# Kernel tuning notes

Hardware: AMD Instinct MI355X
Metric: run time of the kernel (lower is better)

The kernel has to match this reference:

```python
import jax, jax.numpy as jnp
import numpy as np

D_MODEL = 1024
N_HEADS = 16
D_K = D_MODEL // N_HEADS
LOCAL_WINDOW = 128
GLOBAL_TOKENS = 16


def sparse_mask(seq_len):
    i = jnp.arange(seq_len)[:, None]
    j = jnp.arange(seq_len)[None, :]
    local = jnp.abs(i - j) <= LOCAL_WINDOW
    glob = (i < GLOBAL_TOKENS) | (j < GLOBAL_TOKENS)
    causal = j <= i
    return ((local | glob) & causal)[None, None]  # [1,1,S,S]


def setup_inputs() -> dict:
    key = jax.random.key(0)
    ks = jax.random.split(key, 11)
    B, S = 2, 2048
    std = 1.0 / np.sqrt(D_MODEL)
    inp = {
        'query': jax.random.normal(ks[0], (B, S, D_MODEL), jnp.float32),
        'key': jax.random.normal(ks[1], (B, S, D_MODEL), jnp.float32),
        'value': jax.random.normal(ks[2], (B, S, D_MODEL), jnp.float32),
        'w_q': jax.random.normal(ks[3], (D_MODEL, D_MODEL), jnp.float32) * std,
        'b_q': jnp.zeros((D_MODEL,), jnp.float32),
        'w_k': jax.random.normal(ks[4], (D_MODEL, D_MODEL), jnp.float32) * std,
        'b_k': jnp.zeros((D_MODEL,), jnp.float32),
        'w_v': jax.random.normal(ks[5], (D_MODEL, D_MODEL), jnp.float32) * std,
        'b_v': jnp.zeros((D_MODEL,), jnp.float32),
        'w_o': jax.random.normal(ks[6], (D_MODEL, D_MODEL), jnp.float32) * std,
        'b_o': jnp.zeros((D_MODEL,), jnp.float32),
    }
    return inp


def reference(query, key, value, w_q, b_q, w_k, b_k, w_v, b_v, w_o, b_o):
    B, S, _ = query.shape
    # project and split heads -> [B,H,S,d_k]
    def proj(x, w, b):
        y = x @ w.T + b
        return y.reshape(B, S, N_HEADS, D_K).transpose(0, 2, 1, 3)
    q = proj(query, w_q, b_q)
    k = proj(key, w_k, b_k)
    v = proj(value, w_v, b_v)
    scores = jnp.einsum('bhqd,bhkd->bhqk', q, k) / np.sqrt(D_K).astype(np.float32)
    mask = sparse_mask(S)
    scores = jnp.where(mask, scores, -jnp.inf)
    attn = jax.nn.softmax(scores, axis=-1)
    out = jnp.einsum('bhqk,bhkd->bhqd', attn, v)
    out = out.transpose(0, 2, 1, 3).reshape(B, S, D_MODEL)
    return out @ w_o.T + b_o
```

## Files before the change

### kernel.cpp

```cpp
#include <hip/hip_runtime.h>

typedef unsigned short u16;
typedef u16 u16x8 __attribute__((ext_vector_type(8)));
typedef __bf16 bf16x8 __attribute__((ext_vector_type(8)));
typedef float f32x4 __attribute__((ext_vector_type(4)));

#define MFMA16 __builtin_amdgcn_mfma_f32_16x16x32_bf16

__device__ __forceinline__ u16 f2bf(float f) {
  unsigned u = __builtin_bit_cast(unsigned, f);
  u += 0x7FFFu + ((u >> 16) & 1u);
  return (u16)(u >> 16);
}

__device__ __forceinline__ int swz(int row, int bcol) {
  return row * 128 + (bcol ^ ((row & 7) << 4));
}

__device__ __forceinline__ void gl16(const u16* g, u16* l) {
  __builtin_amdgcn_global_load_lds(
      (const __attribute__((address_space(1))) unsigned int*)g,
      (__attribute__((address_space(3))) unsigned int*)l, 16, 0, 0);
}

__device__ __forceinline__ void BARR() {
  asm volatile("" ::: "memory");
  __builtin_amdgcn_s_barrier();
  asm volatile("" ::: "memory");
}
#define VMCNT(n) asm volatile("s_waitcnt vmcnt(" #n ")" ::: "memory")

__global__ __launch_bounds__(256)
void cast7(const float* __restrict__ a0, const float* __restrict__ a1,
           const float* __restrict__ a2, const float* __restrict__ a3,
           const float* __restrict__ a4, const float* __restrict__ a5,
           const float* __restrict__ a6, u16* __restrict__ ws) {
  const int y = blockIdx.y;
  const float* s;
  u16* d;
  int n;
  switch (y) {
    case 0: s = a0; d = ws + 4194304; n = 4194304; break;
    case 1: s = a1; d = ws + 8388608; n = 4194304; break;
    case 2: s = a2; d = ws + 12582912; n = 4194304; break;
    case 3: s = a3; d = ws + 0; n = 1048576; break;
    case 4: s = a4; d = ws + 1048576; n = 1048576; break;
    case 5: s = a5; d = ws + 2097152; n = 1048576; break;
    default: s = a6; d = ws + 3145728; n = 1048576; break;
  }
  const int i = (blockIdx.x * 256 + threadIdx.x) * 8;
  if (i >= n) return;
  float4 v0 = *(const float4*)(s + i);
  float4 v1 = *(const float4*)(s + i + 4);
  u16x8 p = {f2bf(v0.x), f2bf(v0.y), f2bf(v0.z), f2bf(v0.w),
             f2bf(v1.x), f2bf(v1.y), f2bf(v1.z), f2bf(v1.w)};
  *(u16x8*)(d + i) = p;
}

#define STGA(tt, c)                                                         \
  gl16(A + (m0 + (c)*64 + (w << 3) + (lane >> 3)) * 1024 + (tt)*64 +        \
           (((lane & 7) ^ (lane >> 3)) << 3),                               \
       (u16*)(sb + (((tt)&1) << 16) + (c)*8192 + (w << 10)))
#define STGB(tt, c)                                                         \
  gl16(B + (n0 + (c)*64 + (w << 3) + (lane >> 3)) * 1024 + (tt)*64 +        \
           (((lane & 7) ^ (lane >> 3)) << 3),                               \
       (u16*)(sb + (((tt)&1) << 16) + 32768 + (c)*8192 + (w << 10)))

__global__ __launch_bounds__(512)
void qkv_gemm256(const u16* __restrict__ ws_in, const float* __restrict__ c0,
                 const float* __restrict__ c1, const float* __restrict__ c2,
                 u16* __restrict__ o0, u16* __restrict__ o1,
                 u16* __restrict__ o2) {
  const int bid = blockIdx.x;
  const int s = (bid & 7) * 24 + (bid >> 3);
  const int z = s >> 6;
  const int rem = s & 63;
  const int m0 = (rem >> 2) << 8;
  const int n0 = (rem & 3) << 8;

  const u16* __restrict__ A = ws_in + 4194304 + z * 4194304;
  const u16* __restrict__ B = ws_in + z * 1048576;
  const float* Bi = (z == 0) ? c0 : (z == 1) ? c1 : c2;
  u16* O = (z == 0) ? o0 : (z == 1) ? o1 : o2;

  const int tid = threadIdx.x, lane = tid & 63, w = tid >> 6;
  const int wm = w >> 2, wn = w & 3;
  const int r = lane & 15, g = lane >> 4;

  __shared__ u16 SH[65536];
  char* sb = (char*)SH;

  f32x4 acc[8][4] = {};
  bf16x8 af[2][4], bf[2][4];

  const int colr0 = (g * 16) ^ ((r & 7) << 4);
  const int colr1 = (64 + g * 16) ^ ((r & 7) << 4);
  const int rowAb = (wm * 128 + r) * 128;
  const int rowBb = 32768 + (wn * 64 + r) * 128;

#define LDA(half)                                                           \
  _Pragma("unroll") for (int m = 0; m < 4; ++m) {                           \
    char* p = sb + bo + rowAb + ((half)*64 + m * 16) * 128;                 \
    af[0][m] = __builtin_bit_cast(bf16x8, *(const u16x8*)(p + colr0));      \
    af[1][m] = __builtin_bit_cast(bf16x8, *(const u16x8*)(p + colr1));      \
  }
#define LDB(n)                                                              \
  {                                                                         \
    char* p = sb + bo + rowBb + (n)*16 * 128;                               \
    bf[0][n] = __builtin_bit_cast(bf16x8, *(const u16x8*)(p + colr0));      \
    bf[1][n] = __builtin_bit_cast(bf16x8, *(const u16x8*)(p + colr1));      \
  }
#define FMAH(h)                                                             \
  __builtin_amdgcn_s_setprio(1);                                            \
  _Pragma("unroll") for (int m = 0; m < 4; ++m)                             \
  _Pragma("unroll") for (int n = 0; n < 4; ++n) {                           \
    acc[(h)*4 + m][n] = MFMA16(af[0][m], bf[0][n], acc[(h)*4 + m][n], 0, 0, \
                               0);                                          \
    acc[(h)*4 + m][n] = MFMA16(af[1][m], bf[1][n], acc[(h)*4 + m][n], 0, 0, \
                               0);                                          \
  }                                                                         \
  __builtin_amdgcn_s_setprio(0);

#pragma unroll
  for (int c = 0; c < 4; ++c) STGB(0, c);
#pragma unroll
  for (int c = 0; c < 4; ++c) STGA(0, c);
  VMCNT(0);
  __builtin_amdgcn_s_barrier();
  asm volatile("" ::: "memory");

  for (int t = 0; t < 16; ++t) {
    const int bo = (t & 1) << 16;
    if (t < 15) { STGB(t + 1, 0); STGB(t + 1, 1); STGB(t + 1, 2); STGB(t + 1, 3); }
    LDA(0);
    LDB(0); LDB(1); LDB(2); LDB(3);
    FMAH(0);
    if (t < 15) { VMCNT(4); } else { VMCNT(0); }
    BARR();
    if (t < 15) { STGA(t + 1, 0); STGA(t + 1, 2); STGA(t + 1, 1); STGA(t + 1, 3); }
    LDA(1);
    FMAH(1);
    if (t < 15) { VMCNT(2); }
    BARR();
  }

#pragma unroll
  for (int n = 0; n < 4; ++n) {
    const int gn = n0 + wn * 64 + n * 16 + r;
    const int hh = gn >> 6, d = gn & 63;
    const float bv = Bi[gn];
#pragma unroll
    for (int m = 0; m < 8; ++m) {
#pragma unroll
      for (int q = 0; q < 4; ++q) {
        int gm = m0 + wm * 128 + m * 16 + g * 4 + q;
        int bb = gm >> 11, sIdx = gm & 2047;
        O[((bb * 16 + hh) * 2048 + sIdx) * 64 + d] = f2bf(acc[m][n][q] + bv);
      }
    }
  }
#undef LDA
#undef LDB
#undef FMAH
}

#define OSTGA(tt, c, j)                                                     \
  gl16(Ain + (m0 + (c)*64 + (w << 4) + (j)*8 + (lane >> 3)) * 1024 +        \
           (tt)*64 + (((lane & 7) ^ (lane >> 3)) << 3),                     \
       (u16*)(sb + (((tt)&1) << 15) + (c)*8192 + (w << 11) + ((j) << 10)))
#define OSTGB(tt, c, j)                                                     \
  gl16(W + (n0 + (c)*64 + (w << 4) + (j)*8 + (lane >> 3)) * 1024 +          \
           (tt)*64 + (((lane & 7) ^ (lane >> 3)) << 3),                     \
       (u16*)(sb + (((tt)&1) << 15) + 16384 + (c)*8192 + (w << 11) +        \
              ((j) << 10)))

__global__ __launch_bounds__(256)
void out_gemm_p(const u16* __restrict__ Ain, const u16* __restrict__ W,
                const float* __restrict__ Bi, float* __restrict__ C) {
  const int bid = blockIdx.x;
  const int s = (bid & 7) * 32 + (bid >> 3);
  const int m0 = (s >> 3) << 7, n0 = (s & 7) << 7;

  const int tid = threadIdx.x, lane = tid & 63, w = tid >> 6;
  const int wm = w >> 1, wn = w & 1;
  const int r = lane & 15, g = lane >> 4;

  __shared__ u16 SH[32768];
  char* sb = (char*)SH;

  f32x4 acc[4][4] = {};
  bf16x8 af[2][4], bf[2][4];

  const int colr0 = (g * 16) ^ ((r & 7) << 4);
  const int colr1 = (64 + g * 16) ^ ((r & 7) << 4);
  const int rowAb = (wm * 64 + r) * 128;
  const int rowBb = 16384 + (wn * 64 + r) * 128;

#define OLDA()                                                              \
  _Pragma("unroll") for (int m = 0; m < 4; ++m) {                           \
    char* p = sb + bo + rowAb + m * 16 * 128;                               \
    af[0][m] = __builtin_bit_cast(bf16x8, *(const u16x8*)(p + colr0));      \
    af[1][m] = __builtin_bit_cast(bf16x8, *(const u16x8*)(p + colr1));      \
  }
#define OLDB(n)                                                             \
  {                                                                         \
    char* p = sb + bo + rowBb + (n)*16 * 128;                               \
    bf[0][n] = __builtin_bit_cast(bf16x8, *(const u16x8*)(p + colr0));      \
    bf[1][n] = __builtin_bit_cast(bf16x8, *(const u16x8*)(p + colr1));      \
  }
#define OFMA(nh)                                                            \
  __builtin_amdgcn_s_setprio(1);                                            \
  _Pragma("unroll") for (int m = 0; m < 4; ++m)                             \
  _Pragma("unroll") for (int n = 0; n < 2; ++n) {                           \
    acc[m][(nh)*2 + n] =                                                    \
        MFMA16(af[0][m], bf[0][(nh)*2 + n], acc[m][(nh)*2 + n], 0, 0, 0);   \
    acc[m][(nh)*2 + n] =                                                    \
        MFMA16(af[1][m], bf[1][(nh)*2 + n], acc[m][(nh)*2 + n], 0, 0, 0);   \
  }                                                                         \
  __builtin_amdgcn_s_setprio(0);

#pragma unroll
  for (int c = 0; c < 2; ++c) { OSTGA(0, c, 0); OSTGA(0, c, 1); }
#pragma unroll
  for (int c = 0; c < 2; ++c) { OSTGB(0, c, 0); OSTGB(0, c, 1); }
#pragma unroll
  for (int c = 0; c < 2; ++c) { OSTGA(1, c, 0); OSTGA(1, c, 1); }
  VMCNT(4);
  __builtin_amdgcn_s_barrier();
  asm volatile("" ::: "memory");

  for (int t = 0; t < 16; ++t) {
    const int bo = (t & 1) << 15;
    if (t < 15) { OSTGB(t + 1, 0, 0); OSTGB(t + 1, 0, 1); OSTGB(t + 1, 1, 0); OSTGB(t + 1, 1, 1); }
    OLDA();
    OLDB(0); OLDB(1);
    OFMA(0);
    BARR();
    if (t < 14) { OSTGA(t + 2, 0, 0); OSTGA(t + 2, 0, 1); OSTGA(t + 2, 1, 0); OSTGA(t + 2, 1, 1); }
    OLDB(2); OLDB(3);
    OFMA(1);
    if (t < 14) { VMCNT(4); } else if (t == 14) { VMCNT(0); }
    BARR();
  }

#pragma unroll
  for (int m = 0; m < 4; ++m) {
#pragma unroll
    for (int n = 0; n < 4; ++n) {
      int gn = n0 + wn * 64 + n * 16 + r;
      float bv = Bi[gn];
#pragma unroll
      for (int q = 0; q < 4; ++q) {
        int gm = m0 + wm * 64 + m * 16 + g * 4 + q;
        C[gm * 1024 + gn] = acc[m][n][q] + bv;
      }
    }
  }
#undef OLDA
#undef OLDB
#undef OFMA
}

__global__ __launch_bounds__(256)
void attn_kernel(const u16* __restrict__ Q, const u16* __restrict__ K,
                 const u16* __restrict__ V, u16* __restrict__ O) {
  const int qt = blockIdx.x, h = blockIdx.y, b = blockIdx.z;
  const int tid = threadIdx.x, lane = tid & 63, w = tid >> 6;
  const int r = lane & 15, g = lane >> 4;
  const int q0 = qt * 64;
  const int base = (b * 16 + h) * 131072;
  const u16* Qb = Q + base;
  const u16* Kb = K + base;
  const u16* Vb = V + base;

  __shared__ u16 Ks[64 * 64];
  __shared__ u16 Vt[64 * 64];
  __shared__ u16 Pl[4608];

  bf16x8 qf[2];
  {
    const u16* qp = Qb + (q0 + w * 16 + r) * 64 + g * 8;
    qf[0] = __builtin_bit_cast(bf16x8, *(const u16x8*)qp);
    qf[1] = __builtin_bit_cast(bf16x8, *(const u16x8*)(qp + 32));
  }

  f32x4 acc[4] = {};
  float m_run[4] = {-1e30f, -1e30f, -1e30f, -1e30f};
  float l_run[4] = {};

  const int nt = (qt <= 3) ? (qt + 1) : 4;
  const int srow = tid >> 3, sc = (tid & 7) * 8;

  for (int tix = 0; tix < nt; ++tix) {
    const int t = (tix == 0) ? 0 : ((qt <= 3) ? tix : (qt - 3 + tix));
    const int j0 = t * 64;
    __syncthreads();
#pragma unroll
    for (int i = 0; i < 2; ++i) {
      int row = i * 32 + srow;
      u16x8 kv = *(const u16x8*)(Kb + (j0 + row) * 64 + sc);
      *(u16x8*)((char*)Ks + swz(row, sc * 2)) = kv;
      u16x8 vv = *(const u16x8*)(Vb + (j0 + row) * 64 + sc);
#pragma unroll
      for (int qq = 0; qq < 8; ++qq) {
        int d = sc + qq;
        *(u16*)((char*)Vt + d * 128 + ((2 * row) ^ ((d & 7) << 4))) = vv[qq];
      }
    }
    __syncthreads();

    f32x4 S[4] = {};
#pragma unroll
    for (int kk = 0; kk < 2; ++kk)
#pragma unroll
      for (int n = 0; n < 4; ++n) {
        bf16x8 kf = __builtin_bit_cast(
            bf16x8,
            *(const u16x8*)((char*)Ks + swz(n * 16 + r, kk * 64 + g * 16)));
        S[n] = MFMA16(qf[kk], kf, S[n], 0, 0, 0);
      }

    float mloc[4] = {-1e30f, -1e30f, -1e30f, -1e30f};
#pragma unroll
    for (int n = 0; n < 4; ++n) {
      int j = j0 + n * 16 + r;
#pragma unroll
      for (int q = 0; q < 4; ++q) {
        int i = q0 + w * 16 + g * 4 + q;
        bool ok = (j <= i) && (((i - j) <= 128) || (j < 16));
        float s = ok ? S[n][q] * 0.125f : -1e30f;
        S[n][q] = s;
        mloc[q] = fmaxf(mloc[q], s);
      }
    }
#pragma unroll
    for (int q = 0; q < 4; ++q)
#pragma unroll
      for (int off = 1; off < 16; off <<= 1)
        mloc[q] = fmaxf(mloc[q], __shfl_xor(mloc[q], off));

    float alpha[4], rsum[4] = {};
#pragma unroll
    for (int q = 0; q < 4; ++q) {
      float mn = fmaxf(m_run[q], mloc[q]);
      alpha[q] = __expf(m_run[q] - mn);
      m_run[q] = mn;
    }
#pragma unroll
    for (int n = 0; n < 4; ++n)
#pragma unroll
      for (int q = 0; q < 4; ++q) {
        float p = __expf(S[n][q] - m_run[q]);
        S[n][q] = p;
        rsum[q] += p;
      }
#pragma unroll
    for (int q = 0; q < 4; ++q) {
#pragma unroll
      for (int off = 1; off < 16; off <<= 1)
        rsum[q] += __shfl_xor(rsum[q], off);
      l_run[q] = l_run[q] * alpha[q] + rsum[q];
    }
#pragma unroll
    for (int n = 0; n < 4; ++n) {
      acc[n][0] *= alpha[0];
      acc[n][1] *= alpha[1];
      acc[n][2] *= alpha[2];
      acc[n][3] *= alpha[3];
    }

#pragma unroll
    for (int n = 0; n < 4; ++n)
#pragma unroll
      for (int q = 0; q < 4; ++q)
        *((u16*)((char*)Pl + w * 2304 + (g * 4 + q) * 144) + (n * 16 + r)) =
            f2bf(S[n][q]);

#pragma unroll
    for (int kk = 0; kk < 2; ++kk) {
      bf16x8 pf = __builtin_bit_cast(
          bf16x8,
          *(const u16x8*)((char*)Pl + w * 2304 + r * 144 + kk * 64 + g * 16));
#pragma unroll
      for (int n = 0; n < 4; ++n) {
        bf16x8 vf = __builtin_bit_cast(
            bf16x8,
            *(const u16x8*)((char*)Vt + swz(n * 16 + r, kk * 64 + g * 16)));
        acc[n] = MFMA16(pf, vf, acc[n], 0, 0, 0);
      }
    }
  }

#pragma unroll
  for (int n = 0; n < 4; ++n)
#pragma unroll
    for (int q = 0; q < 4; ++q) {
      int s = q0 + w * 16 + g * 4 + q;
      int d = n * 16 + r;
      O[(b * 2048 + s) * 1024 + h * 64 + d] = f2bf(acc[n][q] / l_run[q]);
    }
}

extern "C" void kernel_launch(void* const* d_in, const int* in_sizes, int n_in,
                              void* d_out, int out_size, void* d_ws,
                              size_t ws_size, hipStream_t stream) {
  const float* b_q = (const float*)d_in[4];
  const float* b_k = (const float*)d_in[6];
  const float* b_v = (const float*)d_in[8];
  const float* b_o = (const float*)d_in[10];

  u16* ws = (u16*)d_ws;
  u16* Qw = ws + 16777216;
  u16* Kw = ws + 20971520;
  u16* Vw = ws + 25165824;
  u16* Aw = ws + 4194304;

  cast7<<<dim3(2048, 7), dim3(256), 0, stream>>>(
      (const float*)d_in[0], (const float*)d_in[1], (const float*)d_in[2],
      (const float*)d_in[3], (const float*)d_in[5], (const float*)d_in[7],
      (const float*)d_in[9], ws);
  qkv_gemm256<<<dim3(192), dim3(512), 0, stream>>>(ws, b_q, b_k, b_v, Qw, Kw,
                                                   Vw);
  attn_kernel<<<dim3(32, 16, 2), dim3(256), 0, stream>>>(Qw, Kw, Vw, Aw);
  out_gemm_p<<<dim3(256), dim3(256), 0, stream>>>(Aw, ws + 3145728, b_o,
                                                  (float*)d_out);
}
```

Measured before the change: 96.04 us.

## Switch QKV GEMM to shared 128x128 tile core and flatten cast grid

Replaces the 256x256-tile, 512-thread QKV projection GEMM with a 128x128-tile, 256-thread kernel that reuses the output-projection GEMM's inner loop, now factored into a shared core128 function. The launch grows from 192 to 768 blocks, which should fill the MI355X's compute units better and allow more than one block per CU, since each block uses half the LDS. The trade-off is lower data reuse per tile, so global and L2 traffic go up. The cast kernel also moves to a flat 1D grid, which removes the idle threads the old version had in the weight-matrix rows.

```diff
diff --git a/kernel.cpp b/kernel.cpp
--- a/kernel.cpp
+++ b/kernel.cpp
@@ -31,137 +31,30 @@
 #define VMCNT(n) asm volatile("s_waitcnt vmcnt(" #n ")" ::: "memory")
 
 __global__ __launch_bounds__(256)
-void cast7(const float* __restrict__ a0, const float* __restrict__ a1,
-           const float* __restrict__ a2, const float* __restrict__ a3,
-           const float* __restrict__ a4, const float* __restrict__ a5,
-           const float* __restrict__ a6, u16* __restrict__ ws) {
-  const int y = blockIdx.y;
+void cast_all(const float* __restrict__ q, const float* __restrict__ k,
+              const float* __restrict__ v, const float* __restrict__ wq,
+              const float* __restrict__ wk, const float* __restrict__ wv,
+              const float* __restrict__ wo, u16* __restrict__ ws) {
+  const long i = ((long)blockIdx.x * 256 + threadIdx.x) * 8;
   const float* s;
   u16* d;
-  int n;
-  switch (y) {
-    case 0: s = a0; d = ws + 4194304; n = 4194304; break;
-    case 1: s = a1; d = ws + 8388608; n = 4194304; break;
-    case 2: s = a2; d = ws + 12582912; n = 4194304; break;
-    case 3: s = a3; d = ws + 0; n = 1048576; break;
-    case 4: s = a4; d = ws + 1048576; n = 1048576; break;
-    case 5: s = a5; d = ws + 2097152; n = 1048576; break;
-    default: s = a6; d = ws + 3145728; n = 1048576; break;
-  }
-  const int i = (blockIdx.x * 256 + threadIdx.x) * 8;
-  if (i >= n) return;
-  float4 v0 = *(const float4*)(s + i);
-  float4 v1 = *(const float4*)(s + i + 4);
+  if (i < 12582912) {
+    const int seg = (int)(i >> 22);
+    const float* xs = (seg == 0) ? q : (seg == 1) ? k : v;
+    s = xs + (i & 4194303);
+    d = ws + 4194304 + i;
+  } else {
+    const long j = i - 12582912;
+    const int seg = (int)(j >> 20);
+    const float* wsrc = (seg == 0) ? wq : (seg == 1) ? wk : (seg == 2) ? wv : wo;
+    s = wsrc + (j & 1048575);
+    d = ws + j;
+  }
+  float4 v0 = *(const float4*)s;
+  float4 v1 = *(const float4*)(s + 4);
   u16x8 p = {f2bf(v0.x), f2bf(v0.y), f2bf(v0.z), f2bf(v0.w),
              f2bf(v1.x), f2bf(v1.y), f2bf(v1.z), f2bf(v1.w)};
-  *(u16x8*)(d + i) = p;
-}
-
-#define STGA(tt, c)                                                         \
-  gl16(A + (m0 + (c)*64 + (w << 3) + (lane >> 3)) * 1024 + (tt)*64 +        \
-           (((lane & 7) ^ (lane >> 3)) << 3),                               \
-       (u16*)(sb + (((tt)&1) << 16) + (c)*8192 + (w << 10)))
-#define STGB(tt, c)                                                         \
-  gl16(B + (n0 + (c)*64 + (w << 3) + (lane >> 3)) * 1024 + (tt)*64 +        \
-           (((lane & 7) ^ (lane >> 3)) << 3),                               \
-       (u16*)(sb + (((tt)&1) << 16) + 32768 + (c)*8192 + (w << 10)))
-
-__global__ __launch_bounds__(512)
-void qkv_gemm256(const u16* __restrict__ ws_in, const float* __restrict__ c0,
-                 const float* __restrict__ c1, const float* __restrict__ c2,
-                 u16* __restrict__ o0, u16* __restrict__ o1,
-                 u16* __restrict__ o2) {
-  const int bid = blockIdx.x;
-  const int s = (bid & 7) * 24 + (bid >> 3);
-  const int z = s >> 6;
-  const int rem = s & 63;
-  const int m0 = (rem >> 2) << 8;
-  const int n0 = (rem & 3) << 8;
-
-  const u16* __restrict__ A = ws_in + 4194304 + z * 4194304;
-  const u16* __restrict__ B = ws_in + z * 1048576;
-  const float* Bi = (z == 0) ? c0 : (z == 1) ? c1 : c2;
-  u16* O = (z == 0) ? o0 : (z == 1) ? o1 : o2;
-
-  const int tid = threadIdx.x, lane = tid & 63, w = tid >> 6;
-  const int wm = w >> 2, wn = w & 3;
-  const int r = lane & 15, g = lane >> 4;
-
-  __shared__ u16 SH[65536];
-  char* sb = (char*)SH;
-
-  f32x4 acc[8][4] = {};
-  bf16x8 af[2][4], bf[2][4];
-
-  const int colr0 = (g * 16) ^ ((r & 7) << 4);
-  const int colr1 = (64 + g * 16) ^ ((r & 7) << 4);
-  const int rowAb = (wm * 128 + r) * 128;
-  const int rowBb = 32768 + (wn * 64 + r) * 128;
-
-#define LDA(half)                                                           \
-  _Pragma("unroll") for (int m = 0; m < 4; ++m) {                           \
-    char* p = sb + bo + rowAb + ((half)*64 + m * 16) * 128;                 \
-    af[0][m] = __builtin_bit_cast(bf16x8, *(const u16x8*)(p + colr0));      \
-    af[1][m] = __builtin_bit_cast(bf16x8, *(const u16x8*)(p + colr1));      \
-  }
-#define LDB(n)                                                              \
-  {                                                                         \
-    char* p = sb + bo + rowBb + (n)*16 * 128;                               \
-    bf[0][n] = __builtin_bit_cast(bf16x8, *(const u16x8*)(p + colr0));      \
-    bf[1][n] = __builtin_bit_cast(bf16x8, *(const u16x8*)(p + colr1));      \
-  }
-#define FMAH(h)                                                             \
-  __builtin_amdgcn_s_setprio(1);                                            \
-  _Pragma("unroll") for (int m = 0; m < 4; ++m)                             \
-  _Pragma("unroll") for (int n = 0; n < 4; ++n) {                           \
-    acc[(h)*4 + m][n] = MFMA16(af[0][m], bf[0][n], acc[(h)*4 + m][n], 0, 0, \
-                               0);                                          \
-    acc[(h)*4 + m][n] = MFMA16(af[1][m], bf[1][n], acc[(h)*4 + m][n], 0, 0, \
-                               0);                                          \
-  }                                                                         \
-  __builtin_amdgcn_s_setprio(0);
-
-#pragma unroll
-  for (int c = 0; c < 4; ++c) STGB(0, c);
-#pragma unroll
-  for (int c = 0; c < 4; ++c) STGA(0, c);
-  VMCNT(0);
-  __builtin_amdgcn_s_barrier();
-  asm volatile("" ::: "memory");
-
-  for (int t = 0; t < 16; ++t) {
-    const int bo = (t & 1) << 16;
-    if (t < 15) { STGB(t + 1, 0); STGB(t + 1, 1); STGB(t + 1, 2); STGB(t + 1, 3); }
-    LDA(0);
-    LDB(0); LDB(1); LDB(2); LDB(3);
-    FMAH(0);
-    if (t < 15) { VMCNT(4); } else { VMCNT(0); }
-    BARR();
-    if (t < 15) { STGA(t + 1, 0); STGA(t + 1, 2); STGA(t + 1, 1); STGA(t + 1, 3); }
-    LDA(1);
-    FMAH(1);
-    if (t < 15) { VMCNT(2); }
-    BARR();
-  }
-
-#pragma unroll
-  for (int n = 0; n < 4; ++n) {
-    const int gn = n0 + wn * 64 + n * 16 + r;
-    const int hh = gn >> 6, d = gn & 63;
-    const float bv = Bi[gn];
-#pragma unroll
-    for (int m = 0; m < 8; ++m) {
-#pragma unroll
-      for (int q = 0; q < 4; ++q) {
-        int gm = m0 + wm * 128 + m * 16 + g * 4 + q;
-        int bb = gm >> 11, sIdx = gm & 2047;
-        O[((bb * 16 + hh) * 2048 + sIdx) * 64 + d] = f2bf(acc[m][n][q] + bv);
-      }
-    }
-  }
-#undef LDA
-#undef LDB
-#undef FMAH
+  *(u16x8*)d = p;
 }
 
 #define OSTGA(tt, c, j)                                                     \
@@ -173,29 +66,6 @@
            (tt)*64 + (((lane & 7) ^ (lane >> 3)) << 3),                     \
        (u16*)(sb + (((tt)&1) << 15) + 16384 + (c)*8192 + (w << 11) +        \
               ((j) << 10)))
-
-__global__ __launch_bounds__(256)
-void out_gemm_p(const u16* __restrict__ Ain, const u16* __restrict__ W,
-                const float* __restrict__ Bi, float* __restrict__ C) {
-  const int bid = blockIdx.x;
-  const int s = (bid & 7) * 32 + (bid >> 3);
-  const int m0 = (s >> 3) << 7, n0 = (s & 7) << 7;
-
-  const int tid = threadIdx.x, lane = tid & 63, w = tid >> 6;
-  const int wm = w >> 1, wn = w & 1;
-  const int r = lane & 15, g = lane >> 4;
-
-  __shared__ u16 SH[32768];
-  char* sb = (char*)SH;
-
-  f32x4 acc[4][4] = {};
-  bf16x8 af[2][4], bf[2][4];
-
-  const int colr0 = (g * 16) ^ ((r & 7) << 4);
-  const int colr1 = (64 + g * 16) ^ ((r & 7) << 4);
-  const int rowAb = (wm * 64 + r) * 128;
-  const int rowBb = 16384 + (wn * 64 + r) * 128;
-
 #define OLDA()                                                              \
   _Pragma("unroll") for (int m = 0; m < 4; ++m) {                           \
     char* p = sb + bo + rowAb + m * 16 * 128;                               \
@@ -218,6 +88,20 @@
         MFMA16(af[1][m], bf[1][(nh)*2 + n], acc[m][(nh)*2 + n], 0, 0, 0);   \
   }                                                                         \
   __builtin_amdgcn_s_setprio(0);
+
+__device__ __forceinline__ void core128(const u16* __restrict__ Ain,
+                                        const u16* __restrict__ W, int m0,
+                                        int n0, char* sb,
+                                        f32x4 (&acc)[4][4]) {
+  const int tid = threadIdx.x, lane = tid & 63, w = tid >> 6;
+  const int wm = w >> 1, wn = w & 1;
+  const int r = lane & 15, g = lane >> 4;
+  bf16x8 af[2][4], bf[2][4];
+
+  const int colr0 = (g * 16) ^ ((r & 7) << 4);
+  const int colr1 = (64 + g * 16) ^ ((r & 7) << 4);
+  const int rowAb = (wm * 64 + r) * 128;
+  const int rowBb = 16384 + (wn * 64 + r) * 128;
 
 #pragma unroll
   for (int c = 0; c < 2; ++c) { OSTGA(0, c, 0); OSTGA(0, c, 1); }
@@ -242,6 +126,63 @@
     if (t < 14) { VMCNT(4); } else if (t == 14) { VMCNT(0); }
     BARR();
   }
+}
+
+__global__ __launch_bounds__(256)
+void qkv_gemm128(const u16* __restrict__ ws_in, const float* __restrict__ c0,
+                 const float* __restrict__ c1, const float* __restrict__ c2,
+                 u16* __restrict__ o0, u16* __restrict__ o1,
+                 u16* __restrict__ o2) {
+  const int bid = blockIdx.x;
+  const int s = (bid & 7) * 96 + (bid >> 3);
+  const int z = s >> 8;
+  const int rem = s & 255;
+  const int m0 = (rem >> 3) << 7, n0 = (rem & 7) << 7;
+
+  const u16* __restrict__ Ain = ws_in + 4194304 + z * 4194304;
+  const u16* __restrict__ W = ws_in + z * 1048576;
+  const float* Bi = (z == 0) ? c0 : (z == 1) ? c1 : c2;
+  u16* O = (z == 0) ? o0 : (z == 1) ? o1 : o2;
+
+  const int tid = threadIdx.x, lane = tid & 63, w = tid >> 6;
+  const int wm = w >> 1, wn = w & 1;
+  const int r = lane & 15, g = lane >> 4;
+
+  __shared__ u16 SH[32768];
+  f32x4 acc[4][4] = {};
+  core128(Ain, W, m0, n0, (char*)SH, acc);
+
+#pragma unroll
+  for (int n = 0; n < 4; ++n) {
+    const int gn = n0 + wn * 64 + n * 16 + r;
+    const int hh = gn >> 6, d = gn & 63;
+    const float bv = Bi[gn];
+#pragma unroll
+    for (int m = 0; m < 4; ++m) {
+#pragma unroll
+      for (int q = 0; q < 4; ++q) {
+        int gm = m0 + wm * 64 + m * 16 + g * 4 + q;
+        int bb = gm >> 11, sIdx = gm & 2047;
+        O[((bb * 16 + hh) * 2048 + sIdx) * 64 + d] = f2bf(acc[m][n][q] + bv);
+      }
+    }
+  }
+}
+
+__global__ __launch_bounds__(256)
+void out_gemm_p(const u16* __restrict__ Ain2, const u16* __restrict__ W2,
+                const float* __restrict__ Bi, float* __restrict__ C) {
+  const int bid = blockIdx.x;
+  const int s = (bid & 7) * 32 + (bid >> 3);
+  const int m0 = (s >> 3) << 7, n0 = (s & 7) << 7;
+
+  const int tid = threadIdx.x, lane = tid & 63, w = tid >> 6;
+  const int wm = w >> 1, wn = w & 1;
+  const int r = lane & 15, g = lane >> 4;
+
+  __shared__ u16 SH[32768];
+  f32x4 acc[4][4] = {};
+  core128(Ain2, W2, m0, n0, (char*)SH, acc);
 
 #pragma unroll
   for (int m = 0; m < 4; ++m) {
@@ -256,9 +197,6 @@
       }
     }
   }
-#undef OLDA
-#undef OLDB
-#undef OFMA
 }
 
 __global__ __launch_bounds__(256)
@@ -415,11 +353,11 @@
   u16* Vw = ws + 25165824;
   u16* Aw = ws + 4194304;
 
-  cast7<<<dim3(2048, 7), dim3(256), 0, stream>>>(
+  cast_all<<<dim3(8192), dim3(256), 0, stream>>>(
       (const float*)d_in[0], (const float*)d_in[1], (const float*)d_in[2],
       (const float*)d_in[3], (const float*)d_in[5], (const float*)d_in[7],
       (const float*)d_in[9], ws);
-  qkv_gemm256<<<dim3(192), dim3(512), 0, stream>>>(ws, b_q, b_k, b_v, Qw, Kw,
+  qkv_gemm128<<<dim3(768), dim3(256), 0, stream>>>(ws, b_q, b_k, b_v, Qw, Kw,
                                                    Vw);
   attn_kernel<<<dim3(32, 16, 2), dim3(256), 0, stream>>>(Qw, Kw, Vw, Aw);
   out_gemm_p<<<dim3(256), dim3(256), 0, stream>>>(Aw, ws + 3145728, b_o,
```

After: 93.16 us. -3.0%, faster.
